# Performance work log

Hardware: AMD Instinct MI355X
Metric: run time of the kernel (lower is better)

Reference implementation:

```python
import jax, jax.numpy as jnp
import numpy as np

N_TOKENS = 4096
HIDDEN = 1024
N_EXPERTS = 8
TOP_K = 2
EXPANDED = 2048


def setup_inputs() -> dict:
    key = jax.random.key(0)
    ks = jax.random.split(key, 4)
    tokens = jax.random.normal(ks[0], (N_TOKENS, HIDDEN), dtype=jnp.float32)
    router_w = jax.random.normal(ks[1], (N_EXPERTS, HIDDEN), dtype=jnp.float32) * (1.0 / np.sqrt(HIDDEN))
    router_b = jnp.zeros((N_EXPERTS,), dtype=jnp.float32)
    w1 = jax.random.normal(ks[2], (N_EXPERTS, HIDDEN, EXPANDED), dtype=jnp.float32) * (1.0 / np.sqrt(HIDDEN))
    b1 = jnp.zeros((N_EXPERTS, EXPANDED), dtype=jnp.float32)
    w2 = jax.random.normal(ks[3], (N_EXPERTS, EXPANDED, HIDDEN), dtype=jnp.float32) * (1.0 / np.sqrt(EXPANDED))
    b2 = jnp.zeros((N_EXPERTS, HIDDEN), dtype=jnp.float32)
    return {"tokens": tokens, "router_w": router_w, "router_b": router_b,
            "w1": w1, "b1": b1, "w2": w2, "b2": b2}


def reference(tokens, router_w, router_b, w1, b1, w2, b2):
    # Router: logits [N, E], top-k scores -> softmax over the k selected experts.
    logits = tokens @ router_w.T + router_b
    top_scores, expert_ids = jax.lax.top_k(logits, TOP_K)      # [N, K]
    probs = jax.nn.softmax(top_scores, axis=-1)                # [N, K]

    # Instead of gathering full per-token weight matrices (as the torch code does),
    # run each expert's dense MLP over all tokens and combine with the per-token
    # routing weight for that expert. Identical math: each token's contribution is
    # sum_k probs[n,k] * MLP_{expert_ids[n,k]}(tokens[n]).
    out = jnp.zeros_like(tokens)
    for e in range(N_EXPERTS):
        h = jax.nn.gelu(tokens @ w1[e] + b1[e], approximate=False)  # [N, EXPANDED]
        o = h @ w2[e] + b2[e]                                       # [N, HIDDEN]
        # Combined routing weight for expert e (top_k indices are distinct).
        gate = jnp.sum(jnp.where(expert_ids == e, probs, 0.0), axis=-1)  # [N]
        out = out + gate[:, None] * o
    return out
```

## Files before the change

kernel.cpp:

```cpp
#include <hip/hip_runtime.h>
#include <hip/hip_bf16.h>

typedef unsigned short u16;
typedef __attribute__((ext_vector_type(8))) short short8;
typedef __attribute__((ext_vector_type(4))) float f32x4;

#define N_TOKENS 4096
#define HIDDEN   1024
#define N_EXP    8
#define EXPAND   2048

#define TOKB_OFF  0ull
#define W1T_OFF   8388608ull
#define OBUF_OFF  8388608ull
#define W2T_OFF   41943040ull
#define H_OFF     75497472ull
#define RLT_OFF   109051904ull
#define RLG_OFF   109084672ull
#define CNT_OFF   109117440ull
#define E01_OFF   109117472ull
#define GATE_OFF  109183008ull
#define ROWS2_OFF 109215776ull
#define BCNT_OFF  109248544ull
#define OBASE_OFF 109249568ull

__device__ __forceinline__ u16 f2bf(float f) {
  union { float f; unsigned u; } v; v.f = f;
  unsigned r = v.u + 0x7fffu + ((v.u >> 16) & 1u);
  return (u16)(r >> 16);
}

__device__ __forceinline__ float bf2f(u16 b) {
  union { unsigned u; float f; } v; v.u = ((unsigned)b) << 16;
  return v.f;
}

__device__ __forceinline__ void glds16(const void* g, void* l) {
  __builtin_amdgcn_global_load_lds(
      (const __attribute__((address_space(1))) void*)g,
      (__attribute__((address_space(3))) void*)l, 16, 0, 0);
}

__device__ __forceinline__ float gelu_tanh(float x) {
  float u = x * (0.7978845608f + 0.0356774081f * x * x);
  float t = __expf(-2.0f * fabsf(u));
  float th = (1.0f - t) / (1.0f + t);
  th = (u >= 0.0f) ? th : -th;
  return 0.5f * x * (1.0f + th);
}

__global__ __launch_bounds__(256) void prep_k(const float* __restrict__ w1,
                                              u16* __restrict__ w1t,
                                              const float* __restrict__ w2,
                                              u16* __restrict__ w2t,
                                              const float* __restrict__ tokens,
                                              const float* __restrict__ rw,
                                              const float* __restrict__ rb,
                                              u16* __restrict__ tokb,
                                              int* __restrict__ e01,
                                              float* __restrict__ gates) {
  __shared__ __align__(16) char smem[32768];
  int x = blockIdx.x;
  int tid = threadIdx.x;

  if (x >= 1024) {
    u16 (*t)[66] = (u16 (*)[66])smem;
    int idx = x - 1024;
    const float* in; u16* out; int R, C, cx, ry, e;
    if (idx < 4096) {
      e = idx >> 9; int rem = idx & 511;
      cx = rem & 31; ry = rem >> 5;
      in = w1; out = w1t; R = HIDDEN; C = EXPAND;
    } else {
      int id2 = idx - 4096;
      e = id2 >> 9; int rem = id2 & 511;
      cx = rem & 15; ry = rem >> 4;
      in = w2; out = w2t; R = EXPAND; C = HIDDEN;
    }
    int c0 = cx * 64, r0 = ry * 64;
    const float* ip = in + (size_t)e * R * C;
    u16* op = out + (size_t)e * R * C;
    #pragma unroll
    for (int i = 0; i < 16; ++i) {
      int flat = i * 256 + tid;
      int row = flat >> 6, col = flat & 63;
      t[row][col] = f2bf(ip[(size_t)(r0 + row) * C + c0 + col]);
    }
    __syncthreads();
    #pragma unroll
    for (int i = 0; i < 16; ++i) {
      int flat = i * 256 + tid;
      int orow = flat >> 6, ocol = flat & 63;
      op[(size_t)(c0 + orow) * R + r0 + ocol] = t[ocol][orow];
    }
    return;
  }

  float* rwl = (float*)smem;
  for (int i = tid; i < N_EXP * HIDDEN / 4; i += 256)
    ((float4*)rwl)[i] = ((const float4*)rw)[i];
  __syncthreads();
  int w = tid >> 6, l = tid & 63;
  int t = x * 4 + w;
  const float* tp = tokens + (size_t)t * HIDDEN;
  u16* tb = tokb + (size_t)t * HIDDEN;
  float acc[8] = {0.f,0.f,0.f,0.f,0.f,0.f,0.f,0.f};
  #pragma unroll
  for (int it = 0; it < 4; ++it) {
    int k = it * 256 + l * 4;
    float4 tv = *(const float4*)&tp[k];
    ushort4 o;
    o.x = f2bf(tv.x); o.y = f2bf(tv.y); o.z = f2bf(tv.z); o.w = f2bf(tv.w);
    *(ushort4*)&tb[k] = o;
    #pragma unroll
    for (int e = 0; e < 8; ++e) {
      const float4 rv = *(const float4*)&rwl[e * HIDDEN + k];
      acc[e] += tv.x * rv.x + tv.y * rv.y + tv.z * rv.z + tv.w * rv.w;
    }
  }
  #pragma unroll
  for (int off = 32; off >= 1; off >>= 1) {
    #pragma unroll
    for (int e = 0; e < 8; ++e) acc[e] += __shfl_xor(acc[e], off);
  }
  if (l == 0) {
    float lg[8];
    #pragma unroll
    for (int e = 0; e < 8; ++e) lg[e] = acc[e] + rb[e];
    int b0 = 0; float v0 = lg[0];
    #pragma unroll
    for (int e = 1; e < 8; ++e) if (lg[e] > v0) { v0 = lg[e]; b0 = e; }
    int b1 = -1; float v1 = -3.4e38f;
    #pragma unroll
    for (int e = 0; e < 8; ++e) {
      if (e == b0) continue;
      if (lg[e] > v1) { v1 = lg[e]; b1 = e; }
    }
    float d = expf(v1 - v0);
    float p1 = d / (1.f + d);
    float p0 = 1.f - p1;
    e01[t * 2] = b0;   e01[t * 2 + 1] = b1;
    gates[t * 2] = p0; gates[t * 2 + 1] = p1;
  }
}

__global__ __launch_bounds__(256) void sortcnt_k(const int* __restrict__ e01,
                                                 int* __restrict__ bcnt) {
  __shared__ int wc[4][8];
  int b = blockIdx.x, tid = threadIdx.x, w = tid >> 6, l = tid & 63;
  int ei = e01[b * 256 + tid];
  #pragma unroll
  for (int e = 0; e < 8; ++e) {
    unsigned long long m = __ballot(ei == e);
    if (l == 0) wc[w][e] = __popcll(m);
  }
  __syncthreads();
  if (tid < 8)
    bcnt[tid * 32 + b] = wc[0][tid] + wc[1][tid] + wc[2][tid] + wc[3][tid];
}

__global__ void scan_k(const int* __restrict__ bcnt,
                       int* __restrict__ obase, int* __restrict__ cnt) {
  if (threadIdx.x == 0) {
    int ec[8];
    for (int e = 0; e < 8; ++e) {
      int s = 0;
      for (int b = 0; b < 32; ++b) { obase[e * 32 + b] = s; s += bcnt[e * 32 + b]; }
      ec[e] = s; cnt[e] = s;
    }
    int base = 0;
    for (int e = 0; e < 8; ++e) {
      for (int b = 0; b < 32; ++b) obase[e * 32 + b] += base;
      base += ec[e];
    }
  }
}

__global__ __launch_bounds__(256) void scatter_k(const int* __restrict__ e01,
                                                 const float* __restrict__ gates,
                                                 const int* __restrict__ obase,
                                                 int* __restrict__ rlt,
                                                 float* __restrict__ rlg,
                                                 int* __restrict__ rows2) {
  __shared__ int wc[4][8];
  __shared__ int wpre[4][8];
  int b = blockIdx.x, tid = threadIdx.x, w = tid >> 6, l = tid & 63;
  int i = b * 256 + tid;
  int ei = e01[i];
  unsigned long long ltm = (1ull << l) - 1ull;
  int lanerank = 0;
  #pragma unroll
  for (int e = 0; e < 8; ++e) {
    unsigned long long m = __ballot(ei == e);
    if (l == 0) wc[w][e] = __popcll(m);
    if (ei == e) lanerank = __popcll(m & ltm);
  }
  __syncthreads();
  if (tid < 8) {
    int s = 0;
    for (int ww = 0; ww < 4; ++ww) { wpre[ww][tid] = s; s += wc[ww][tid]; }
  }
  __syncthreads();
  int row = obase[ei * 32 + b] + wpre[w][ei] + lanerank;
  rlt[row] = i >> 1;
  rlg[row] = gates[i];
  rows2[i] = row;
}


#define STAGE(Ad, Bd, KT) {                                                      \
  glds16(ga[0] + (size_t)(KT) * 64, &Ad[threadIdx.x * 8]);                       \
  glds16(ga[1] + (size_t)(KT) * 64, &Ad[(512 + threadIdx.x) * 8]);               \
  glds16(gb0   + (size_t)(KT) * 64, &Bd[threadIdx.x * 8]);                       \
}

#define GEMM_TILE(As, Bs) {                                                      \
  _Pragma("unroll") for (int kk = 0; kk < 2; ++kk) {                             \
    short8 afr[2], bfr[2];                                                       \
    _Pragma("unroll") for (int i = 0; i < 2; ++i) {                              \
      afr[i] = *(const short8*)&As[oa[kk][i]];                                   \
      bfr[i] = *(const short8*)&Bs[ob[kk][i]];                                   \
    }                                                                            \
    _Pragma("unroll") for (int i = 0; i < 2; ++i)                                \
      _Pragma("unroll") for (int j = 0; j < 2; ++j)                              \
        acc[i][j] = __builtin_amdgcn_mfma_f32_16x16x32_bf16(                     \
            afr[i], bfr[j], acc[i][j], 0, 0, 0);                                 \
  }                                                                              \
}

#define FRAG_OFFSETS {                                                           \
  _Pragma("unroll") for (int kk = 0; kk < 2; ++kk) {                             \
    int cc = kk * 4 + lg;                                                        \
    _Pragma("unroll") for (int i = 0; i < 2; ++i) {                              \
      int Ra = wr * 32 + i * 16 + lr;                                            \
      oa[kk][i] = Ra * 64 + (cc ^ (Ra & 7)) * 8;                                 \
      int Rb = wc * 32 + i * 16 + lr;                                            \
      ob[kk][i] = Rb * 64 + (cc ^ (Rb & 7)) * 8;                                 \
    }                                                                            \
  }                                                                              \
}

__global__ __launch_bounds__(512) void ffn1_k(const u16* __restrict__ tok,
                                              const u16* __restrict__ w1t,
                                              const float* __restrict__ b1,
                                              const int* __restrict__ rlt,
                                              const int* __restrict__ cnt,
                                              u16* __restrict__ h) {
  __shared__ __align__(16) short A0[8192];
  __shared__ __align__(16) short A1[8192];
  __shared__ __align__(16) short B0[4096];
  __shared__ __align__(16) short B1[4096];

  int tid = threadIdx.x, w = tid >> 6, l = tid & 63;
  int wr = w >> 1, wc = w & 1;
  int lr = l & 15, lg = l >> 4;
  int oa[2][2], ob[2][2];
  FRAG_OFFSETS

  int e = blockIdx.x & 7;
  int rnk = blockIdx.x >> 3;
  int estr = gridDim.x >> 3;
  int m0 = 0;
  #pragma unroll
  for (int i = 0; i < 8; ++i) { int ci = cnt[i]; if (i < e) m0 += ci; }
  int ne = cnt[e];
  int mts = (ne + 127) >> 7;
  int NT_e = mts * (EXPAND / 64);

  for (int r = rnk; r < NT_e; r += estr) {
    int mt = r >> 5, nt = r & 31;
    int m0g = m0 + mt * 128;
    int mrem = ne - mt * 128;

    const u16* ga[2]; const u16* gb0;
    #pragma unroll
    for (int c = 0; c < 2; ++c) {
      int flat = c * 512 + tid, rih = flat >> 3;
      int ch = (flat & 7) ^ (rih & 7);
      int tokid = rlt[m0g + ((rih < mrem) ? rih : 0)];
      ga[c] = tok + (size_t)tokid * HIDDEN + ch * 8;
    }
    {
      int rih = tid >> 3;
      int ch = (tid & 7) ^ (rih & 7);
      int nrow = nt * 64 + rih;
      gb0 = w1t + (size_t)e * (EXPAND * HIDDEN) + (size_t)nrow * HIDDEN + ch * 8;
    }

    f32x4 acc[2][2] = {};
    STAGE(A0, B0, 0)
    __syncthreads();
    #pragma unroll 1
    for (int it = 0; it < 8; ++it) {
      STAGE(A1, B1, 2 * it + 1)
      GEMM_TILE(A0, B0)
      __syncthreads();
      if (it < 7) STAGE(A0, B0, 2 * it + 2)
      GEMM_TILE(A1, B1)
      __syncthreads();
    }

    #pragma unroll
    for (int i = 0; i < 2; ++i) {
      #pragma unroll
      for (int rr = 0; rr < 4; ++rr) {
        int row = wr * 32 + i * 16 + lg * 4 + rr;
        if (row >= mrem) continue;
        size_t hrow = (size_t)(m0g + row) * EXPAND;
        #pragma unroll
        for (int j = 0; j < 2; ++j) {
          int col = nt * 64 + wc * 32 + j * 16 + lr;
          float x = acc[i][j][rr] + b1[e * EXPAND + col];
          h[hrow + col] = f2bf(gelu_tanh(x));
        }
      }
    }
  }
}

__global__ __launch_bounds__(512) void ffn2_k(const u16* __restrict__ h,
                                              const u16* __restrict__ w2t,
                                              const float* __restrict__ b2,
                                              const float* __restrict__ rlg,
                                              const int* __restrict__ cnt,
                                              u16* __restrict__ obuf) {
  __shared__ __align__(16) short A0[8192];
  __shared__ __align__(16) short A1[8192];
  __shared__ __align__(16) short B0[4096];
  __shared__ __align__(16) short B1[4096];

  int tid = threadIdx.x, w = tid >> 6, l = tid & 63;
  int wr = w >> 1, wc = w & 1;
  int lr = l & 15, lg = l >> 4;
  int oa[2][2], ob[2][2];
  FRAG_OFFSETS

  int e = blockIdx.x & 7;
  int rnk = blockIdx.x >> 3;
  int estr = gridDim.x >> 3;
  int m0 = 0;
  #pragma unroll
  for (int i = 0; i < 8; ++i) { int ci = cnt[i]; if (i < e) m0 += ci; }
  int ne = cnt[e];
  int mts = (ne + 127) >> 7;
  int NT_e = mts * (HIDDEN / 64);

  for (int r = rnk; r < NT_e; r += estr) {
    int mt = r >> 4, nt = r & 15;
    int m0g = m0 + mt * 128;
    int mrem = ne - mt * 128;

    const u16* ga[2]; const u16* gb0;
    #pragma unroll
    for (int c = 0; c < 2; ++c) {
      int flat = c * 512 + tid, rih = flat >> 3;
      int ch = (flat & 7) ^ (rih & 7);
      int rowg = m0g + ((rih < mrem) ? rih : 0);
      ga[c] = h + (size_t)rowg * EXPAND + ch * 8;
    }
    {
      int rih = tid >> 3;
      int ch = (tid & 7) ^ (rih & 7);
      int nrow = nt * 64 + rih;
      gb0 = w2t + (size_t)e * (HIDDEN * EXPAND) + (size_t)nrow * EXPAND + ch * 8;
    }

    f32x4 acc[2][2] = {};
    STAGE(A0, B0, 0)
    __syncthreads();
    #pragma unroll 1
    for (int it = 0; it < 16; ++it) {
      STAGE(A1, B1, 2 * it + 1)
      GEMM_TILE(A0, B0)
      __syncthreads();
      if (it < 15) STAGE(A0, B0, 2 * it + 2)
      GEMM_TILE(A1, B1)
      __syncthreads();
    }

    #pragma unroll
    for (int i = 0; i < 2; ++i) {
      #pragma unroll
      for (int rr = 0; rr < 4; ++rr) {
        int row = wr * 32 + i * 16 + lg * 4 + rr;
        if (row >= mrem) continue;
        float gate = rlg[m0g + row];
        size_t orow = (size_t)(m0g + row) * HIDDEN;
        #pragma unroll
        for (int j = 0; j < 2; ++j) {
          int col = nt * 64 + wc * 32 + j * 16 + lr;
          obuf[orow + col] = f2bf((acc[i][j][rr] + b2[e * HIDDEN + col]) * gate);
        }
      }
    }
  }
}

__global__ __launch_bounds__(256) void combine_k(const u16* __restrict__ obuf,
                                                 const int* __restrict__ rows2,
                                                 float* __restrict__ out) {
  int t = blockIdx.x, c = threadIdx.x;
  int r0 = rows2[t * 2], r1 = rows2[t * 2 + 1];
  ushort4 a = ((const ushort4*)obuf)[(size_t)r0 * 256 + c];
  ushort4 b = ((const ushort4*)obuf)[(size_t)r1 * 256 + c];
  float4 o;
  o.x = bf2f(a.x) + bf2f(b.x);
  o.y = bf2f(a.y) + bf2f(b.y);
  o.z = bf2f(a.z) + bf2f(b.z);
  o.w = bf2f(a.w) + bf2f(b.w);
  ((float4*)out)[(size_t)t * 256 + c] = o;
}

extern "C" void kernel_launch(void* const* d_in, const int* in_sizes, int n_in,
                              void* d_out, int out_size, void* d_ws, size_t ws_size,
                              hipStream_t stream) {
  const float* tokens   = (const float*)d_in[0];
  const float* router_w = (const float*)d_in[1];
  const float* router_b = (const float*)d_in[2];
  const float* w1       = (const float*)d_in[3];
  const float* b1       = (const float*)d_in[4];
  const float* w2       = (const float*)d_in[5];
  const float* b2       = (const float*)d_in[6];
  float* out = (float*)d_out;

  char* ws = (char*)d_ws;
  u16*   tokb  = (u16*)(ws + TOKB_OFF);
  u16*   w1t   = (u16*)(ws + W1T_OFF);
  u16*   obuf  = (u16*)(ws + OBUF_OFF);
  u16*   w2t   = (u16*)(ws + W2T_OFF);
  u16*   h     = (u16*)(ws + H_OFF);
  int*   rlt   = (int*)(ws + RLT_OFF);
  float* rlg   = (float*)(ws + RLG_OFF);
  int*   cnt   = (int*)(ws + CNT_OFF);
  int*   e01   = (int*)(ws + E01_OFF);
  float* gates = (float*)(ws + GATE_OFF);
  int*   rows2 = (int*)(ws + ROWS2_OFF);
  int*   bcnt  = (int*)(ws + BCNT_OFF);
  int*   obase = (int*)(ws + OBASE_OFF);

  prep_k<<<9216, 256, 0, stream>>>(w1, w1t, w2, w2t,
                                   tokens, router_w, router_b, tokb, e01, gates);
  sortcnt_k<<<32, 256, 0, stream>>>(e01, bcnt);
  scan_k<<<1, 64, 0, stream>>>(bcnt, obase, cnt);
  scatter_k<<<32, 256, 0, stream>>>(e01, gates, obase, rlt, rlg, rows2);
  ffn1_k<<<2048, 512, 0, stream>>>(tokb, w1t, b1, rlt, cnt, h);
  ffn2_k<<<1024, 512, 0, stream>>>(h, w2t, b2, rlg, cnt, obuf);
  combine_k<<<N_TOKENS, 256, 0, stream>>>(obuf, rows2, out);
}
```

Measured before the change: 193.7 us.

## Move w2 transpose/convert into ffn1 launch to overlap with GEMM

The fp32-to-bf16 transpose of w2 moves out of the prep kernel and into extra blocks appended to the ffn1 grid, so that weight conversion can overlap with the first expert GEMM instead of being serialized before routing. The expert stride is hardcoded to 256 so the GEMM blocks keep their original work distribution despite the larger grid. The risk is that the transpose blocks share the grid with GEMM blocks and may delay them, and that occupancy is reduced because the transpose blocks carry the large ffn1 shared-memory footprint.

Result: no change. 191.6 us (median of 2 runs) (-1.1%).

```diff
diff --git a/kernel.cpp b/kernel.cpp
--- a/kernel.cpp
+++ b/kernel.cpp
@@ -51,8 +51,6 @@
 
 __global__ __launch_bounds__(256) void prep_k(const float* __restrict__ w1,
                                               u16* __restrict__ w1t,
-                                              const float* __restrict__ w2,
-                                              u16* __restrict__ w2t,
                                               const float* __restrict__ tokens,
                                               const float* __restrict__ rw,
                                               const float* __restrict__ rb,
@@ -66,20 +64,12 @@
   if (x >= 1024) {
     u16 (*t)[66] = (u16 (*)[66])smem;
     int idx = x - 1024;
-    const float* in; u16* out; int R, C, cx, ry, e;
-    if (idx < 4096) {
-      e = idx >> 9; int rem = idx & 511;
-      cx = rem & 31; ry = rem >> 5;
-      in = w1; out = w1t; R = HIDDEN; C = EXPAND;
-    } else {
-      int id2 = idx - 4096;
-      e = id2 >> 9; int rem = id2 & 511;
-      cx = rem & 15; ry = rem >> 4;
-      in = w2; out = w2t; R = EXPAND; C = HIDDEN;
-    }
+    int e = idx >> 9; int rem = idx & 511;
+    int cx = rem & 31, ry = rem >> 5;
+    const int R = HIDDEN, C = EXPAND;
     int c0 = cx * 64, r0 = ry * 64;
-    const float* ip = in + (size_t)e * R * C;
-    u16* op = out + (size_t)e * R * C;
+    const float* ip = w1 + (size_t)e * R * C;
+    u16* op = w1t + (size_t)e * R * C;
     #pragma unroll
     for (int i = 0; i < 16; ++i) {
       int flat = i * 256 + tid;
@@ -245,13 +235,42 @@
                                               const float* __restrict__ b1,
                                               const int* __restrict__ rlt,
                                               const int* __restrict__ cnt,
-                                              u16* __restrict__ h) {
+                                              u16* __restrict__ h,
+                                              const float* __restrict__ w2,
+                                              u16* __restrict__ w2t) {
   __shared__ __align__(16) short A0[8192];
   __shared__ __align__(16) short A1[8192];
   __shared__ __align__(16) short B0[4096];
   __shared__ __align__(16) short B1[4096];
 
-  int tid = threadIdx.x, w = tid >> 6, l = tid & 63;
+  int tid = threadIdx.x;
+
+  if (blockIdx.x >= 2048) {
+    u16 (*t)[66] = (u16 (*)[66])A0;
+    int idx = blockIdx.x - 2048;
+    int e = idx >> 9; int rem = idx & 511;
+    int cx = rem & 15, ry = rem >> 4;
+    const int R = EXPAND, C = HIDDEN;
+    int c0 = cx * 64, r0 = ry * 64;
+    const float* ip = w2 + (size_t)e * R * C;
+    u16* op = w2t + (size_t)e * R * C;
+    #pragma unroll
+    for (int i = 0; i < 8; ++i) {
+      int flat = i * 512 + tid;
+      int row = flat >> 6, col = flat & 63;
+      t[row][col] = f2bf(ip[(size_t)(r0 + row) * C + c0 + col]);
+    }
+    __syncthreads();
+    #pragma unroll
+    for (int i = 0; i < 8; ++i) {
+      int flat = i * 512 + tid;
+      int orow = flat >> 6, ocol = flat & 63;
+      op[(size_t)(c0 + orow) * R + r0 + ocol] = t[ocol][orow];
+    }
+    return;
+  }
+
+  int w = tid >> 6, l = tid & 63;
   int wr = w >> 1, wc = w & 1;
   int lr = l & 15, lg = l >> 4;
   int oa[2][2], ob[2][2];
@@ -259,7 +278,7 @@
 
   int e = blockIdx.x & 7;
   int rnk = blockIdx.x >> 3;
-  int estr = gridDim.x >> 3;
+  const int estr = 256;
   int m0 = 0;
   #pragma unroll
   for (int i = 0; i < 8; ++i) { int ci = cnt[i]; if (i < e) m0 += ci; }
@@ -438,12 +457,12 @@
   int*   bcnt  = (int*)(ws + BCNT_OFF);
   int*   obase = (int*)(ws + OBASE_OFF);
 
-  prep_k<<<9216, 256, 0, stream>>>(w1, w1t, w2, w2t,
-                                   tokens, router_w, router_b, tokb, e01, gates);
+  prep_k<<<5120, 256, 0, stream>>>(w1, w1t, tokens, router_w, router_b,
+                                   tokb, e01, gates);
   sortcnt_k<<<32, 256, 0, stream>>>(e01, bcnt);
   scan_k<<<1, 64, 0, stream>>>(bcnt, obase, cnt);
   scatter_k<<<32, 256, 0, stream>>>(e01, gates, obase, rlt, rlg, rows2);
-  ffn1_k<<<2048, 512, 0, stream>>>(tokb, w1t, b1, rlt, cnt, h);
+  ffn1_k<<<6144, 512, 0, stream>>>(tokb, w1t, b1, rlt, cnt, h, w2, w2t);
   ffn2_k<<<1024, 512, 0, stream>>>(h, w2t, b2, rlg, cnt, obuf);
   combine_k<<<N_TOKENS, 256, 0, stream>>>(obuf, rows2, out);
 }
```
